# Kernel tuning notes

Measured on AMD Instinct MI355X. Metric: run time of the kernel, lower is better.

The kernel has to match this reference:

```python
import jax, jax.numpy as jnp
import numpy as np

B, S, H, NH = 4, 2048, 1024, 16
DK = H // NH

def setup_inputs() -> dict:
    key = jax.random.key(0)
    ks = jax.random.split(key, 8)
    query = jax.random.normal(ks[0], (B, S, H), dtype=jnp.float32)
    key_t = jax.random.normal(ks[1], (B, S, H), dtype=jnp.float32)
    value = jax.random.normal(ks[2], (B, S, H), dtype=jnp.float32)
    mask = jnp.ones((B, S), dtype=jnp.int32)
    # Linear weights (torch convention: y = x @ W.T + b)
    sc = 1.0 / np.sqrt(H)
    Wq = jax.random.uniform(ks[3], (H, H), jnp.float32, -sc, sc)
    Wk = jax.random.uniform(ks[4], (H, H), jnp.float32, -sc, sc)
    Wv = jax.random.uniform(ks[5], (H, H), jnp.float32, -sc, sc)
    Wo = jax.random.uniform(ks[6], (H, H), jnp.float32, -sc, sc)
    bo = jax.random.uniform(ks[7], (H,), jnp.float32, -sc, sc)
    return {"query": query, "key": key_t, "value": value, "mask": mask,
            "Wq": Wq, "Wk": Wk, "Wv": Wv, "Wo": Wo, "bo": bo}

def reference(query, key, value, mask, Wq, Wk, Wv, Wo, bo):
    # project and split heads: (B,S,H) -> (B,NH,S,DK)
    def split_heads(x, W):
        y = x @ W.T
        return y.reshape(B, S, NH, DK).transpose(0, 2, 1, 3)
    q = split_heads(query, Wq)
    k = split_heads(key, Wk)
    v = split_heads(value, Wv)
    scores = jnp.einsum('bhqd,bhkd->bhqk', q, k) / jnp.sqrt(jnp.float32(DK))
    # outer-product padding mask: (B,S)x(B,S) -> (B,1,S,S)
    m = (mask[:, :, None] * mask[:, None, :])[:, None, :, :]
    scores = jnp.where(m == 0, jnp.float32(-1e9), scores)
    p = jax.nn.softmax(scores, axis=-1)  # dropout off (eval mode)
    x = jnp.einsum('bhqk,bhkd->bhqd', p, v)
    x = x.transpose(0, 2, 1, 3).reshape(B, S, H)
    return x @ Wo.T + bo
```

## Files before the change

kernel.cpp:

```cpp
#include <hip/hip_runtime.h>

typedef unsigned short u16;
typedef __bf16 bf16x8 __attribute__((ext_vector_type(8)));
typedef float f32x4 __attribute__((ext_vector_type(4)));

#if __has_builtin(__builtin_amdgcn_exp2f)
#define EXP2(x) __builtin_amdgcn_exp2f(x)
#else
#define EXP2(x) exp2f(x)
#endif

__device__ __forceinline__ u16 f2bf(float f) {
    unsigned u = __float_as_uint(f);
    u += 0x7fffu + ((u >> 16) & 1u);
    return (u16)(u >> 16);
}

__device__ __forceinline__ void gll16(const void* g, void* l) {
    __builtin_amdgcn_global_load_lds(
        (const __attribute__((address_space(1))) void*)g,
        (__attribute__((address_space(3))) void*)l, 16, 0, 0);
}

__device__ __forceinline__ void cvt_body(const float* __restrict__ in,
                                         u16* __restrict__ out, int i) {
    float4 v = reinterpret_cast<const float4*>(in)[i];
    unsigned long long pack =
        (unsigned long long)f2bf(v.x) |
        ((unsigned long long)f2bf(v.y) << 16) |
        ((unsigned long long)f2bf(v.z) << 32) |
        ((unsigned long long)f2bf(v.w) << 48);
    reinterpret_cast<unsigned long long*>(out)[i] = pack;
}

__global__ __launch_bounds__(256) void cvt_all(const float* __restrict__ q,
                                               const float* __restrict__ k,
                                               const float* __restrict__ v,
                                               const float* __restrict__ wq,
                                               const float* __restrict__ wk,
                                               const float* __restrict__ wv,
                                               const float* __restrict__ wo,
                                               u16* __restrict__ oq,
                                               u16* __restrict__ ok,
                                               u16* __restrict__ ov,
                                               u16* __restrict__ owq,
                                               u16* __restrict__ owk,
                                               u16* __restrict__ owv,
                                               u16* __restrict__ owo,
                                               int n4, int nw4) {
    int i = blockIdx.x * 256 + threadIdx.x;
    if (i < n4)          cvt_body(q, oq, i);
    else if (i < 2 * n4) cvt_body(k, ok, i - n4);
    else if (i < 3 * n4) cvt_body(v, ov, i - 2 * n4);
    else {
        int j = i - 3 * n4;
        if (j < nw4)          cvt_body(wq, owq, j);
        else if (j < 2 * nw4) cvt_body(wk, owk, j - nw4);
        else if (j < 3 * nw4) cvt_body(wv, owv, j - 2 * nw4);
        else if (j < 4 * nw4) cvt_body(wo, owo, j - 3 * nw4);
    }
}

template<int MODE>
__global__ __launch_bounds__(256) void gemm_bt(const u16* __restrict__ A,
                                               const u16* __restrict__ B,
                                               void* __restrict__ Cv,
                                               const float* __restrict__ bias) {
    constexpr int K = 1024, N = 1024;
    __shared__ __align__(16) u16 As[128 * 64];
    __shared__ __align__(16) u16 Bs[128 * 64];
    const int tid = threadIdx.x;
    const int wv = tid >> 6, lane = tid & 63, g = lane >> 4, li = lane & 15;
    const int row0 = blockIdx.y << 7, col0 = blockIdx.x << 7;
    const int wm = wv >> 1, wn = wv & 1;

    f32x4 acc[4][4] = {};

    for (int k0 = 0; k0 < K; k0 += 64) {
        __syncthreads();
#pragma unroll
        for (int i = 0; i < 4; i++) {
            const int o   = (wv << 12) + (i << 10) + (lane << 4);
            const int row = o >> 7;
            const int cbg = (o & 127) ^ ((row & 7) << 4);
            gll16(A + (size_t)(row0 + row) * K + k0 + (cbg >> 1),
                  (char*)As + (wv << 12) + (i << 10));
        }
#pragma unroll
        for (int i = 0; i < 4; i++) {
            const int o   = (wv << 12) + (i << 10) + (lane << 4);
            const int row = o >> 7;
            const int cbg = (o & 127) ^ ((row & 7) << 4);
            gll16(B + (size_t)(col0 + row) * K + k0 + (cbg >> 1),
                  (char*)Bs + (wv << 12) + (i << 10));
        }
        __syncthreads();

#pragma unroll
        for (int kk = 0; kk < 2; kk++) {
            bf16x8 af[4], bfr[4];
            const int cb = ((kk << 5) + (g << 3)) << 1;
#pragma unroll
            for (int m = 0; m < 4; m++) {
                const int row = (wm << 6) + (m << 4) + li;
                af[m] = *reinterpret_cast<const bf16x8*>(
                    (const char*)As + (row << 7) + (cb ^ ((row & 7) << 4)));
            }
#pragma unroll
            for (int n = 0; n < 4; n++) {
                const int row = (wn << 6) + (n << 4) + li;
                bfr[n] = *reinterpret_cast<const bf16x8*>(
                    (const char*)Bs + (row << 7) + (cb ^ ((row & 7) << 4)));
            }
#pragma unroll
            for (int m = 0; m < 4; m++)
#pragma unroll
                for (int n = 0; n < 4; n++)
                    acc[m][n] = __builtin_amdgcn_mfma_f32_16x16x32_bf16(
                        af[m], bfr[n], acc[m][n], 0, 0, 0);
        }
    }

    if constexpr (MODE == 0 || MODE == 3) {
        constexpr float SC = (MODE == 3) ? 0.180336880f : 1.0f;
        u16* C = (u16*)Cv;
#pragma unroll
        for (int m = 0; m < 4; m++)
#pragma unroll
            for (int n = 0; n < 4; n++)
#pragma unroll
                for (int r = 0; r < 4; r++) {
                    int row = row0 + (wm << 6) + (m << 4) + (g << 2) + r;
                    int col = col0 + (wn << 6) + (n << 4) + li;
                    C[(size_t)row * N + col] = f2bf(acc[m][n][r] * SC);
                }
    } else if constexpr (MODE == 1) {
        float* C = (float*)Cv;
#pragma unroll
        for (int m = 0; m < 4; m++)
#pragma unroll
            for (int n = 0; n < 4; n++)
#pragma unroll
                for (int r = 0; r < 4; r++) {
                    int row = row0 + (wm << 6) + (m << 4) + (g << 2) + r;
                    int col = col0 + (wn << 6) + (n << 4) + li;
                    C[(size_t)row * N + col] = acc[m][n][r] + bias[col];
                }
    } else {
        u16* C = (u16*)Cv;
#pragma unroll
        for (int m = 0; m < 4; m++)
#pragma unroll
            for (int n = 0; n < 4; n++) {
                int srow = row0 + (wm << 6) + (m << 4) + (g << 2);
                int col  = col0 + (wn << 6) + (n << 4) + li;
                int b = srow >> 11, s = srow & 2047;
                int nh = col >> 6, d = col & 63;
                unsigned long long pack =
                    (unsigned long long)f2bf(acc[m][n][0]) |
                    ((unsigned long long)f2bf(acc[m][n][1]) << 16) |
                    ((unsigned long long)f2bf(acc[m][n][2]) << 32) |
                    ((unsigned long long)f2bf(acc[m][n][3]) << 48);
                *reinterpret_cast<unsigned long long*>(
                    C + ((size_t)((b << 4) + nh) * 64 + d) * 2048 + s) = pack;
            }
    }
}

__global__ __launch_bounds__(512, 4) void attn_fwd(const u16* __restrict__ Q,
                                                   const u16* __restrict__ Kp,
                                                   const u16* __restrict__ Vt,
                                                   const int* __restrict__ mask,
                                                   u16* __restrict__ O) {
    constexpr int S = 2048, H = 1024;
    constexpr int K0OFF = 0, K1OFF = 8192, V0OFF = 16384, V1OFF = 24576;
    __shared__ __align__(16) char lds[32768];
    __shared__ int sm_bad;
    const int tid = threadIdx.x, wv = tid >> 6, lane = tid & 63;
    const int g = lane >> 4, li = lane & 15;
    const int bid = blockIdx.x;
    const int swz = ((bid & 7) << 7) + (bid >> 3);
    const int q0 = (swz & 15) << 7, h = (swz >> 4) & 15, b = swz >> 8;
    const char* Kg = (const char*)(Kp + (size_t)b * S * H + h * 64);
    const char* Vg = (const char*)(Vt + (size_t)(b * 16 + h) * 64 * S);

    auto stageK = [&](int koff, int kv2) {
        const int o   = tid << 4;
        const int row = o >> 7;
        const int cbg = (o & 127) ^ ((row & 7) << 4);
        const int gk  = (((row >> 2) & 3) << 4) + ((row >> 4) << 2) + (row & 3);
        gll16(Kg + (size_t)(kv2 + gk) * 2048 + cbg, lds + koff + (wv << 10));
    };
    auto stageV = [&](int voff, int kv2) {
        const int o   = tid << 4;
        const int row = o >> 7;
        const int cbg = (o & 127) ^ ((row & 7) << 4);
        gll16(Vg + (size_t)row * 4096 + kv2 * 2 + cbg, lds + voff + (wv << 10));
    };

    if (tid == 0) sm_bad = 0;
    stageK(K0OFF, 0);
    stageV(V0OFF, 0);
    stageK(K1OFF, 64);

    bf16x8 qf[2];
    {
        const u16* Qrow = Q + (size_t)(b * S + q0 + (wv << 4) + li) * H + h * 64 + (g << 3);
        qf[0] = *reinterpret_cast<const bf16x8*>(Qrow);
        qf[1] = *reinterpret_cast<const bf16x8*>(Qrow + 32);
    }

    int z = 0;
#pragma unroll
    for (int j = 0; j < 4; j++) z |= (mask[b * S + (tid << 2) + j] == 0);
    __syncthreads();
    if (z) sm_bad = 1;

    int offK[2], offV[2];
#pragma unroll
    for (int kk = 0; kk < 2; kk++) {
        offK[kk] = (li << 7) + (((kk << 6) + (g << 4)) ^ ((li & 7) << 4));
        offV[kk] = (li << 7) + (((g << 5) + (kk << 4)) ^ ((li & 7) << 4));
    }

    const f32x4 zero4 = {};
    bf16x8 onesf;
#pragma unroll
    for (int j = 0; j < 8; j++) onesf[j] = (__bf16)1.0f;

    f32x4 scE[4] = {}, scO[4] = {};
    auto QK = [&](int koff, f32x4 (&sc)[4]) {
        __builtin_amdgcn_s_setprio(1);
#pragma unroll
        for (int n = 0; n < 4; n++) {
            bf16x8 kf = *reinterpret_cast<const bf16x8*>(
                lds + koff + offK[0] + (n << 11));
            sc[n] = __builtin_amdgcn_mfma_f32_16x16x32_bf16(kf, qf[0], zero4, 0, 0, 0);
        }
#pragma unroll
        for (int n = 0; n < 4; n++) {
            bf16x8 kf = *reinterpret_cast<const bf16x8*>(
                lds + koff + offK[1] + (n << 11));
            sc[n] = __builtin_amdgcn_mfma_f32_16x16x32_bf16(kf, qf[1], sc[n], 0, 0, 0);
        }
        __builtin_amdgcn_s_setprio(0);
    };

    QK(K0OFF, scE);
    __syncthreads();
    const bool bad = (sm_bad != 0);
    const int  mq  = bad ? mask[b * S + q0 + (wv << 4) + li] : 1;

    f32x4 o_[4] = {};
    f32x4 o_l = {};
    bf16x8 pfE[2], pfO[2];

    auto SM = [&](f32x4 (&sc)[4], bf16x8 (&pf)[2], int kv2) {
        if (bad) {
            const unsigned long long kb = __ballot(mask[b * S + kv2 + lane] != 0);
#pragma unroll
            for (int n = 0; n < 4; n++)
#pragma unroll
                for (int r = 0; r < 4; r++) {
                    const int key = (g << 4) + (n << 2) + r;
                    const bool ok = mq && ((kb >> key) & 1ull);
                    sc[n][r] = ok ? sc[n][r] : -1e9f;
                }
        }
#pragma unroll
        for (int n = 0; n < 4; n++)
#pragma unroll
            for (int r = 0; r < 4; r++)
                sc[n][r] = EXP2(sc[n][r]);
#pragma unroll
        for (int j = 0; j < 4; j++) {
            pf[0][j]     = (__bf16)sc[0][j];
            pf[0][4 + j] = (__bf16)sc[1][j];
            pf[1][j]     = (__bf16)sc[2][j];
            pf[1][4 + j] = (__bf16)sc[3][j];
        }
    };

    auto PV = [&](int voff, bf16x8 (&pf)[2]) {
        __builtin_amdgcn_s_setprio(1);
#pragma unroll
        for (int kk = 0; kk < 2; kk++) {
#pragma unroll
            for (int n = 0; n < 4; n++) {
                bf16x8 vf = *reinterpret_cast<const bf16x8*>(
                    lds + voff + offV[kk] + (n << 11));
                o_[n] = __builtin_amdgcn_mfma_f32_16x16x32_bf16(pf[kk], vf, o_[n], 0, 0, 0);
            }
            o_l = __builtin_amdgcn_mfma_f32_16x16x32_bf16(pf[kk], onesf, o_l, 0, 0, 0);
        }
        __builtin_amdgcn_s_setprio(0);
    };

    for (int kv = 0; kv < S; kv += 128) {
        stageV(V1OFF, kv + 64);
        QK(K1OFF, scO);
        if (kv + 128 < S) stageK(K0OFF, kv + 128);
        SM(scE, pfE, kv);
        PV(V0OFF, pfE);
        __syncthreads();
        if (kv + 128 < S) {
            stageV(V0OFF, kv + 128);
            QK(K0OFF, scE);
        }
        if (kv + 192 < S) stageK(K1OFF, kv + 192);
        SM(scO, pfO, kv + 64);
        PV(V1OFF, pfO);
        __syncthreads();
    }

    float linv[4];
#pragma unroll
    for (int r = 0; r < 4; r++)
        linv[r] = o_l[r] > 0.f ? 1.f / o_l[r] : 0.f;
#pragma unroll
    for (int n = 0; n < 4; n++)
#pragma unroll
        for (int r = 0; r < 4; r++) {
            const int row = q0 + (wv << 4) + (g << 2) + r;
            const int col = (h << 6) + (n << 4) + li;
            O[(size_t)(b * S + row) * H + col] = f2bf(o_[n][r] * linv[r]);
        }
}

extern "C" void kernel_launch(void* const* d_in, const int* in_sizes, int n_in,
                              void* d_out, int out_size, void* d_ws, size_t ws_size,
                              hipStream_t stream) {
    (void)in_sizes; (void)n_in; (void)out_size; (void)ws_size;
    const float* q    = (const float*)d_in[0];
    const float* k    = (const float*)d_in[1];
    const float* v    = (const float*)d_in[2];
    const int*   mask = (const int*)d_in[3];
    const float* Wq   = (const float*)d_in[4];
    const float* Wk   = (const float*)d_in[5];
    const float* Wv   = (const float*)d_in[6];
    const float* Wo   = (const float*)d_in[7];
    const float* bo   = (const float*)d_in[8];

    const size_t NEL = 8192ull * 1024ull;
    const size_t WEL = 1024ull * 1024ull;
    u16* ws  = (u16*)d_ws;
    u16* qb  = ws;
    u16* kb  = ws + NEL;
    u16* vb  = ws + 2 * NEL;
    u16* wqb = ws + 3 * NEL;
    u16* wkb = wqb + WEL;
    u16* wvb = wkb + WEL;
    u16* wob = wvb + WEL;
    u16* Qp  = wob + WEL;

    const int n4  = (int)(NEL / 4);
    const int nw4 = (int)(WEL / 4);
    const int cvt_blocks = (3 * n4 + 4 * nw4 + 255) / 256;
    cvt_all<<<dim3(cvt_blocks), dim3(256), 0, stream>>>(
        q, k, v, Wq, Wk, Wv, Wo, qb, kb, vb, wqb, wkb, wvb, wob, n4, nw4);

    dim3 gg(8, 64), bb(256);
    gemm_bt<3><<<gg, bb, 0, stream>>>(qb, wqb, Qp, nullptr);
    gemm_bt<0><<<gg, bb, 0, stream>>>(kb, wkb, qb, nullptr);
    gemm_bt<2><<<gg, bb, 0, stream>>>(vb, wvb, kb, nullptr);

    attn_fwd<<<dim3(1024), dim3(512), 0, stream>>>(Qp, qb, kb, mask, vb);

    gemm_bt<1><<<gg, bb, 0, stream>>>(vb, wob, (float*)d_out, bo);
}
```

Before: 210.3 us.

## Halve attention block to 4 waves, each handling two query subtiles sharing K/V fragments

```diff
diff --git a/kernel.cpp b/kernel.cpp
--- a/kernel.cpp
+++ b/kernel.cpp
@@ -167,13 +167,12 @@
     }
 }
 
-__global__ __launch_bounds__(512, 4) void attn_fwd(const u16* __restrict__ Q,
+__global__ __launch_bounds__(256, 4) void attn_fwd(const u16* __restrict__ Q,
                                                    const u16* __restrict__ Kp,
                                                    const u16* __restrict__ Vt,
                                                    const int* __restrict__ mask,
                                                    u16* __restrict__ O) {
     constexpr int S = 2048, H = 1024;
-    constexpr int K0OFF = 0, K1OFF = 8192, V0OFF = 16384, V1OFF = 24576;
     __shared__ __align__(16) char lds[32768];
     __shared__ int sm_bad;
     const int tid = threadIdx.x, wv = tid >> 6, lane = tid & 63;
@@ -184,37 +183,44 @@
     const char* Kg = (const char*)(Kp + (size_t)b * S * H + h * 64);
     const char* Vg = (const char*)(Vt + (size_t)(b * 16 + h) * 64 * S);
 
-    auto stageK = [&](int koff, int kv2) {
-        const int o   = tid << 4;
-        const int row = o >> 7;
-        const int cbg = (o & 127) ^ ((row & 7) << 4);
-        const int gk  = (((row >> 2) & 3) << 4) + ((row >> 4) << 2) + (row & 3);
-        gll16(Kg + (size_t)(kv2 + gk) * 2048 + cbg, lds + koff + (wv << 10));
+    auto stageKV = [&](int bufOff, int kv2) {
+#pragma unroll
+        for (int i = 0; i < 2; i++) {
+            const int o   = (wv << 11) + (i << 10) + (lane << 4);
+            const int row = o >> 7;
+            const int cbg = (o & 127) ^ ((row & 7) << 4);
+            const int gk  = (((row >> 2) & 3) << 4) + ((row >> 4) << 2) + (row & 3);
+            gll16(Kg + (size_t)(kv2 + gk) * 2048 + cbg,
+                  lds + bufOff + (wv << 11) + (i << 10));
+            gll16(Vg + (size_t)row * 4096 + kv2 * 2 + cbg,
+                  lds + 16384 + bufOff + (wv << 11) + (i << 10));
+        }
     };
-    auto stageV = [&](int voff, int kv2) {
-        const int o   = tid << 4;
-        const int row = o >> 7;
-        const int cbg = (o & 127) ^ ((row & 7) << 4);
-        gll16(Vg + (size_t)row * 4096 + kv2 * 2 + cbg, lds + voff + (wv << 10));
-    };
 
     if (tid == 0) sm_bad = 0;
-    stageK(K0OFF, 0);
-    stageV(V0OFF, 0);
-    stageK(K1OFF, 64);
-
-    bf16x8 qf[2];
-    {
-        const u16* Qrow = Q + (size_t)(b * S + q0 + (wv << 4) + li) * H + h * 64 + (g << 3);
-        qf[0] = *reinterpret_cast<const bf16x8*>(Qrow);
-        qf[1] = *reinterpret_cast<const bf16x8*>(Qrow + 32);
+    stageKV(0, 0);
+
+    bf16x8 qf[2][2];
+#pragma unroll
+    for (int s = 0; s < 2; s++) {
+        const u16* Qrow = Q + (size_t)(b * S + q0 + (s << 6) + (wv << 4) + li) * H
+                          + h * 64 + (g << 3);
+        qf[s][0] = *reinterpret_cast<const bf16x8*>(Qrow);
+        qf[s][1] = *reinterpret_cast<const bf16x8*>(Qrow + 32);
     }
 
     int z = 0;
 #pragma unroll
-    for (int j = 0; j < 4; j++) z |= (mask[b * S + (tid << 2) + j] == 0);
+    for (int j = 0; j < 8; j++) z |= (mask[b * S + (tid << 3) + j] == 0);
     __syncthreads();
     if (z) sm_bad = 1;
+    __syncthreads();
+    const bool bad = (sm_bad != 0);
+    int mq[2] = {1, 1};
+    if (bad) {
+        mq[0] = mask[b * S + q0 + (wv << 4) + li];
+        mq[1] = mask[b * S + q0 + 64 + (wv << 4) + li];
+    }
 
     int offK[2], offV[2];
 #pragma unroll
@@ -228,103 +234,103 @@
 #pragma unroll
     for (int j = 0; j < 8; j++) onesf[j] = (__bf16)1.0f;
 
-    f32x4 scE[4] = {}, scO[4] = {};
-    auto QK = [&](int koff, f32x4 (&sc)[4]) {
+    f32x4 o_[2][4] = {};
+    f32x4 o_l[2] = {};
+
+    auto tile = [&](int bufOff, int kv2) {
+        f32x4 sc[2][4];
         __builtin_amdgcn_s_setprio(1);
 #pragma unroll
         for (int n = 0; n < 4; n++) {
             bf16x8 kf = *reinterpret_cast<const bf16x8*>(
-                lds + koff + offK[0] + (n << 11));
-            sc[n] = __builtin_amdgcn_mfma_f32_16x16x32_bf16(kf, qf[0], zero4, 0, 0, 0);
+                lds + bufOff + offK[0] + (n << 11));
+            sc[0][n] = __builtin_amdgcn_mfma_f32_16x16x32_bf16(kf, qf[0][0], zero4, 0, 0, 0);
+            sc[1][n] = __builtin_amdgcn_mfma_f32_16x16x32_bf16(kf, qf[1][0], zero4, 0, 0, 0);
         }
 #pragma unroll
         for (int n = 0; n < 4; n++) {
             bf16x8 kf = *reinterpret_cast<const bf16x8*>(
-                lds + koff + offK[1] + (n << 11));
-            sc[n] = __builtin_amdgcn_mfma_f32_16x16x32_bf16(kf, qf[1], sc[n], 0, 0, 0);
+                lds + bufOff + offK[1] + (n << 11));
+            sc[0][n] = __builtin_amdgcn_mfma_f32_16x16x32_bf16(kf, qf[0][1], sc[0][n], 0, 0, 0);
+            sc[1][n] = __builtin_amdgcn_mfma_f32_16x16x32_bf16(kf, qf[1][1], sc[1][n], 0, 0, 0);
+        }
+        __builtin_amdgcn_s_setprio(0);
+
+        if (bad) {
+            const unsigned long long kb = __ballot(mask[b * S + kv2 + lane] != 0);
+#pragma unroll
+            for (int s = 0; s < 2; s++)
+#pragma unroll
+                for (int n = 0; n < 4; n++)
+#pragma unroll
+                    for (int r = 0; r < 4; r++) {
+                        const int key = (g << 4) + (n << 2) + r;
+                        const bool ok = mq[s] && ((kb >> key) & 1ull);
+                        sc[s][n][r] = ok ? sc[s][n][r] : -1e9f;
+                    }
+        }
+
+        bf16x8 pf[2][2];
+#pragma unroll
+        for (int s = 0; s < 2; s++) {
+#pragma unroll
+            for (int n = 0; n < 4; n++)
+#pragma unroll
+                for (int r = 0; r < 4; r++)
+                    sc[s][n][r] = EXP2(sc[s][n][r]);
+#pragma unroll
+            for (int j = 0; j < 4; j++) {
+                pf[s][0][j]     = (__bf16)sc[s][0][j];
+                pf[s][0][4 + j] = (__bf16)sc[s][1][j];
+                pf[s][1][j]     = (__bf16)sc[s][2][j];
+                pf[s][1][4 + j] = (__bf16)sc[s][3][j];
+            }
+        }
+
+        __builtin_amdgcn_s_setprio(1);
+#pragma unroll
+        for (int kk = 0; kk < 2; kk++) {
+#pragma unroll
+            for (int n = 0; n < 4; n++) {
+                bf16x8 vf = *reinterpret_cast<const bf16x8*>(
+                    lds + 16384 + bufOff + offV[kk] + (n << 11));
+                o_[0][n] = __builtin_amdgcn_mfma_f32_16x16x32_bf16(pf[0][kk], vf,
+                                                                   o_[0][n], 0, 0, 0);
+                o_[1][n] = __builtin_amdgcn_mfma_f32_16x16x32_bf16(pf[1][kk], vf,
+                                                                   o_[1][n], 0, 0, 0);
+            }
+            o_l[0] = __builtin_amdgcn_mfma_f32_16x16x32_bf16(pf[0][kk], onesf,
+                                                             o_l[0], 0, 0, 0);
+            o_l[1] = __builtin_amdgcn_mfma_f32_16x16x32_bf16(pf[1][kk], onesf,
+                                                             o_l[1], 0, 0, 0);
         }
         __builtin_amdgcn_s_setprio(0);
     };
 
-    QK(K0OFF, scE);
-    __syncthreads();
-    const bool bad = (sm_bad != 0);
-    const int  mq  = bad ? mask[b * S + q0 + (wv << 4) + li] : 1;
-
-    f32x4 o_[4] = {};
-    f32x4 o_l = {};
-    bf16x8 pfE[2], pfO[2];
-
-    auto SM = [&](f32x4 (&sc)[4], bf16x8 (&pf)[2], int kv2) {
-        if (bad) {
-            const unsigned long long kb = __ballot(mask[b * S + kv2 + lane] != 0);
-#pragma unroll
-            for (int n = 0; n < 4; n++)
-#pragma unroll
-                for (int r = 0; r < 4; r++) {
-                    const int key = (g << 4) + (n << 2) + r;
-                    const bool ok = mq && ((kb >> key) & 1ull);
-                    sc[n][r] = ok ? sc[n][r] : -1e9f;
-                }
-        }
+    for (int kv = 0; kv < S; kv += 128) {
+        stageKV(8192, kv + 64);
+        tile(0, kv);
+        __syncthreads();
+        if (kv + 128 < S) stageKV(0, kv + 128);
+        tile(8192, kv + 64);
+        __syncthreads();
+    }
+
+#pragma unroll
+    for (int s = 0; s < 2; s++) {
+        float linv[4];
+#pragma unroll
+        for (int r = 0; r < 4; r++)
+            linv[r] = o_l[s][r] > 0.f ? 1.f / o_l[s][r] : 0.f;
 #pragma unroll
         for (int n = 0; n < 4; n++)
 #pragma unroll
-            for (int r = 0; r < 4; r++)
-                sc[n][r] = EXP2(sc[n][r]);
-#pragma unroll
-        for (int j = 0; j < 4; j++) {
-            pf[0][j]     = (__bf16)sc[0][j];
-            pf[0][4 + j] = (__bf16)sc[1][j];
-            pf[1][j]     = (__bf16)sc[2][j];
-            pf[1][4 + j] = (__bf16)sc[3][j];
-        }
-    };
-
-    auto PV = [&](int voff, bf16x8 (&pf)[2]) {
-        __builtin_amdgcn_s_setprio(1);
-#pragma unroll
-        for (int kk = 0; kk < 2; kk++) {
-#pragma unroll
-            for (int n = 0; n < 4; n++) {
-                bf16x8 vf = *reinterpret_cast<const bf16x8*>(
-                    lds + voff + offV[kk] + (n << 11));
-                o_[n] = __builtin_amdgcn_mfma_f32_16x16x32_bf16(pf[kk], vf, o_[n], 0, 0, 0);
-            }
-            o_l = __builtin_amdgcn_mfma_f32_16x16x32_bf16(pf[kk], onesf, o_l, 0, 0, 0);
-        }
-        __builtin_amdgcn_s_setprio(0);
-    };
-
-    for (int kv = 0; kv < S; kv += 128) {
-        stageV(V1OFF, kv + 64);
-        QK(K1OFF, scO);
-        if (kv + 128 < S) stageK(K0OFF, kv + 128);
-        SM(scE, pfE, kv);
-        PV(V0OFF, pfE);
-        __syncthreads();
-        if (kv + 128 < S) {
-            stageV(V0OFF, kv + 128);
-            QK(K0OFF, scE);
-        }
-        if (kv + 192 < S) stageK(K1OFF, kv + 192);
-        SM(scO, pfO, kv + 64);
-        PV(V1OFF, pfO);
-        __syncthreads();
-    }
-
-    float linv[4];
-#pragma unroll
-    for (int r = 0; r < 4; r++)
-        linv[r] = o_l[r] > 0.f ? 1.f / o_l[r] : 0.f;
-#pragma unroll
-    for (int n = 0; n < 4; n++)
-#pragma unroll
-        for (int r = 0; r < 4; r++) {
-            const int row = q0 + (wv << 4) + (g << 2) + r;
-            const int col = (h << 6) + (n << 4) + li;
-            O[(size_t)(b * S + row) * H + col] = f2bf(o_[n][r] * linv[r]);
-        }
+            for (int r = 0; r < 4; r++) {
+                const int row = q0 + (s << 6) + (wv << 4) + (g << 2) + r;
+                const int col = (h << 6) + (n << 4) + li;
+                O[(size_t)(b * S + row) * H + col] = f2bf(o_[s][n][r] * linv[r]);
+            }
+    }
 }
 
 extern "C" void kernel_launch(void* const* d_in, const int* in_sizes, int n_in,
@@ -364,7 +370,7 @@
     gemm_bt<0><<<gg, bb, 0, stream>>>(kb, wkb, qb, nullptr);
     gemm_bt<2><<<gg, bb, 0, stream>>>(vb, wvb, kb, nullptr);
 
-    attn_fwd<<<dim3(1024), dim3(512), 0, stream>>>(Qp, qb, kb, mask, vb);
+    attn_fwd<<<dim3(1024), dim3(256), 0, stream>>>(Qp, qb, kb, mask, vb);
 
     gemm_bt<1><<<gg, bb, 0, stream>>>(vb, wob, (float*)d_out, bo);
 }
```

After: 213.9 us. No clear change (+1.7%).
